# Kernel optimization log

Measured on AMD Instinct MI355X. Metric: run time of the kernel, lower is better.

Reference implementation:

```python
import jax, jax.numpy as jnp
import numpy as np

IN_FEATURES = 5000
N0, N1, N2 = 512, 512, 256   # num_nodes
NUM_T = 16                   # num_treatments
BATCH = 16384


def setup_inputs() -> dict:
    key = jax.random.key(0)
    ks = jax.random.split(key, 16)
    s = lambda fan_in: 1.0 / np.sqrt(fan_in)
    inp = {
        "input": jax.random.normal(ks[0], (BATCH, IN_FEATURES), dtype=jnp.float32),
        "treatment_and_dosages": jax.random.uniform(ks[1], (BATCH, NUM_T), dtype=jnp.float32),
        # encoder: in_features -> N0 -> N2 (ReLU, ReLU)
        "enc_w1": jax.random.normal(ks[2], (IN_FEATURES, N0), dtype=jnp.float32) * s(IN_FEATURES),
        "enc_b1": jnp.zeros((N0,), dtype=jnp.float32),
        "enc_w2": jax.random.normal(ks[3], (N0, N2), dtype=jnp.float32) * s(N0),
        "enc_b2": jnp.zeros((N2,), dtype=jnp.float32),
        # per-treatment expert: (N2+1) -> N2, ReLU
        "expert_w": jax.random.normal(ks[4], (NUM_T, N2 + 1, N2), dtype=jnp.float32) * s(N2 + 1),
        "expert_b": jnp.zeros((NUM_T, N2), dtype=jnp.float32),
        # decoder: N2 -> N1 -> N0 -> 2*in_features (ReLU, ReLU, linear)
        "dec_w1": jax.random.normal(ks[5], (N2, N1), dtype=jnp.float32) * s(N2),
        "dec_b1": jnp.zeros((N1,), dtype=jnp.float32),
        "dec_w2": jax.random.normal(ks[6], (N1, N0), dtype=jnp.float32) * s(N1),
        "dec_b2": jnp.zeros((N0,), dtype=jnp.float32),
        "dec_w3": jax.random.normal(ks[7], (N0, 2 * IN_FEATURES), dtype=jnp.float32) * s(N0),
        "dec_b3": jnp.zeros((2 * IN_FEATURES,), dtype=jnp.float32),
    }
    return inp


def reference(input, treatment_and_dosages, enc_w1, enc_b1, enc_w2, enc_b2,
              expert_w, expert_b, dec_w1, dec_b1, dec_w2, dec_b2, dec_w3, dec_b3):
    dim = input.shape[1]
    # routing: argmax over treatment columns
    treatment = jnp.argmax(treatment_and_dosages, axis=1)          # [B] int
    # shared encoder MLP
    h = jax.nn.relu(input @ enc_w1 + enc_b1)                       # [B, N0]
    embedding = jax.nn.relu(h @ enc_w2 + enc_b2)                   # [B, N2]
    # gather each row's own dosage and append as extra feature
    dose = jnp.take_along_axis(treatment_and_dosages, treatment[:, None], axis=1)  # [B,1]
    x = jnp.concatenate([embedding, dose], axis=1)                 # [B, N2+1]
    # run all experts on all tokens (dense grouped GEMM), then select per-row expert.
    # this is the vectorized equivalent of the masked gather / per-treatment MLP /
    # scatter-add loop in the torch code.
    all_out = jax.nn.relu(jnp.einsum('bi,tio->bto', x, expert_w) + expert_b)  # [B,T,N2]
    latent_rep = jnp.take_along_axis(all_out, treatment[:, None, None], axis=1)[:, 0, :]  # [B,N2]
    # decoder MLP
    d = jax.nn.relu(latent_rep @ dec_w1 + dec_b1)
    d = jax.nn.relu(d @ dec_w2 + dec_b2)
    rec = d @ dec_w3 + dec_b3                                      # [B, 2*dim]
    gene_means = rec[:, :dim]
    gene_vars = jax.nn.softplus(rec[:, dim:]) + 0.001
    gene_reconstructions2 = jnp.concatenate([gene_means, gene_vars], axis=1)
    return gene_reconstructions2, latent_rep
```

## Files before the change

kernel.cpp:

```cpp
#include <hip/hip_runtime.h>
#include <cstdint>
#include <cstddef>

#define BATCH    16384
#define INF      5000
#define KPAD_IN  5024
#define N0       512
#define N1       512
#define N2       256
#define NUM_T    16
#define XK       288
#define N3       10000
#define N3PAD    10112

typedef _Float16 f16;
typedef _Float16 f16x8 __attribute__((ext_vector_type(8)));
typedef float    f32x4 __attribute__((ext_vector_type(4)));

typedef __attribute__((address_space(1))) void gvoid;
typedef __attribute__((address_space(3))) void lvoid;

__device__ __forceinline__ void gload_lds16(const void* g, void* l) {
    __builtin_amdgcn_global_load_lds((gvoid*)g, (lvoid*)l, 16, 0, 0);
}

__device__ __forceinline__ float fast_exp2(float x) {
    float r; asm("v_exp_f32 %0, %1" : "=v"(r) : "v"(x)); return r;
}
__device__ __forceinline__ float fast_log2(float x) {
    float r; asm("v_log_f32 %0, %1" : "=v"(r) : "v"(x)); return r;
}
__device__ __forceinline__ float fast_softplus(float v) {
    float t = fast_exp2(-fabsf(v) * 1.44269504f);
    return fmaxf(v, 0.f) + 0.69314718f * fast_log2(1.f + t);
}


__global__ void cast_input_kernel(const float* __restrict__ in, f16* __restrict__ out) {
    int tid = blockIdx.x * 256 + threadIdx.x;
    int r = tid / (KPAD_IN / 8);
    int k = (tid - r * (KPAD_IN / 8)) << 3;
    if (r >= BATCH) return;
    f16x8 v;
#pragma unroll
    for (int j = 0; j < 8; j++) {
        int kk = k + j;
        float x = (kk < INF) ? in[(size_t)r * INF + kk] : 0.f;
        v[j] = (f16)x;
    }
    *(f16x8*)(out + (size_t)r * KPAD_IN + k) = v;
}

__global__ void tcast_kernel(const float* __restrict__ W, f16* __restrict__ Wt,
                             int K, int Nsrc, int Kpad, int Ndst) {
    int tid = blockIdx.x * 256 + threadIdx.x;
    int kb = Kpad >> 3;
    int n = tid / kb;
    int k = (tid - n * kb) << 3;
    if (n >= Ndst) return;
    f16x8 v;
#pragma unroll
    for (int j = 0; j < 8; j++) {
        int kk = k + j;
        float x = (kk < K && n < Nsrc) ? W[(size_t)kk * Nsrc + n] : 0.f;
        v[j] = (f16)x;
    }
    *(f16x8*)(Wt + (size_t)n * Kpad + k) = v;
}

__global__ void tcast_expert_kernel(const float* __restrict__ W, f16* __restrict__ Wt) {
    int tid = blockIdx.x * 256 + threadIdx.x;
    int nt = tid / (XK / 8);
    int k = (tid - nt * (XK / 8)) << 3;
    if (nt >= NUM_T * N2) return;
    int t = nt >> 8, n = nt & 255;
    f16x8 v;
#pragma unroll
    for (int j = 0; j < 8; j++) {
        int kk = k + j;
        float x = (kk < N2 + 1) ? W[((size_t)t * (N2 + 1) + kk) * N2 + n] : 0.f;
        v[j] = (f16)x;
    }
    *(f16x8*)(Wt + ((size_t)t * N2 + n) * XK + k) = v;
}

__global__ void treat_kernel(const float* __restrict__ td, int* __restrict__ treat,
                             f16* __restrict__ xbuf) {
    int b = blockIdx.x * 256 + threadIdx.x;
    if (b >= BATCH) return;
    const float* row = td + (size_t)b * NUM_T;
    float mx = row[0]; int mi = 0;
#pragma unroll
    for (int i = 1; i < NUM_T; i++) {
        float v = row[i];
        if (v > mx) { mx = v; mi = i; }
    }
    treat[b] = mi;
    f16* xr = xbuf + (size_t)b * XK;
    xr[256] = (f16)mx;
#pragma unroll
    for (int i = 257; i < XK; i++) xr[i] = (f16)0.f;
}


enum { EPI_F16 = 0, EPI_EXPERT = 1, EPI_DEC3 = 2 };

template <int EPI>
__global__ __launch_bounds__(256, 2)
void gemm_tpl(const f16* __restrict__ A, const f16* __restrict__ Bt,
              const float* __restrict__ bias, int K,
              f16* __restrict__ out16, int ldo,
              const int* __restrict__ treat, float* __restrict__ outf) {
    __shared__ f16 sA[128 * 32];
    __shared__ f16 sB[128 * 32];
    const int tid  = threadIdx.x;
    const int w    = tid >> 6;
    const int lane = tid & 63;
    const int lr   = lane >> 2;
    const int lc8  = (lane & 3) * 8;
    const int r0   = blockIdx.x * 128;
    const int n0   = blockIdx.y * 128;
    const int expert = (EPI == EPI_EXPERT) ? (int)blockIdx.z : 0;

    const f16* btBase = Bt;
    if (EPI == EPI_EXPERT) btBase += (size_t)expert * N2 * K;

    const f16* a0 = A      + (size_t)(r0 + w * 16 + lr) * K + lc8;
    const f16* a1 = a0 + (size_t)64 * K;
    const f16* b0 = btBase + (size_t)(n0 + w * 16 + lr) * K + lc8;
    const f16* b1 = b0 + (size_t)64 * K;
    f16* sA0 = sA + w * 512;
    f16* sA1 = sA + (w + 4) * 512;
    f16* sB0 = sB + w * 512;
    f16* sB1 = sB + (w + 4) * 512;

    f32x4 acc[4][4];
#pragma unroll
    for (int i = 0; i < 4; i++)
#pragma unroll
        for (int j = 0; j < 4; j++) acc[i][j] = (f32x4){0.f, 0.f, 0.f, 0.f};

    const int wr = (w >> 1) * 64;
    const int wc = (w & 1) * 64;
    const int fm = lane & 15;
    const int fk = (lane >> 4) * 8;

    for (int k0 = 0; k0 < K; k0 += 32) {
        __syncthreads();
        gload_lds16(a0, sA0); gload_lds16(a1, sA1);
        gload_lds16(b0, sB0); gload_lds16(b1, sB1);
        a0 += 32; a1 += 32; b0 += 32; b1 += 32;
        __syncthreads();

        f16x8 af[4], bf[4];
#pragma unroll
        for (int mi = 0; mi < 4; mi++)
            af[mi] = *(const f16x8*)(sA + (wr + mi * 16 + fm) * 32 + fk);
#pragma unroll
        for (int ni = 0; ni < 4; ni++)
            bf[ni] = *(const f16x8*)(sB + (wc + ni * 16 + fm) * 32 + fk);
#pragma unroll
        for (int mi = 0; mi < 4; mi++)
#pragma unroll
            for (int ni = 0; ni < 4; ni++)
                acc[mi][ni] = __builtin_amdgcn_mfma_f32_16x16x32_f16(
                    af[mi], bf[ni], acc[mi][ni], 0, 0, 0);
    }

    const float* bp = (EPI == EPI_EXPERT) ? bias + expert * N2 : bias;
    const int rbase = r0 + wr + ((lane >> 4) << 2);
    const int cbase = n0 + wc + fm;
#pragma unroll
    for (int mi = 0; mi < 4; mi++) {
#pragma unroll
        for (int r = 0; r < 4; r++) {
            int row = rbase + mi * 16 + r;
            if (EPI == EPI_EXPERT) {
                if (treat[row] != expert) continue;
            }
#pragma unroll
            for (int ni = 0; ni < 4; ni++) {
                int col = cbase + ni * 16;
                float v = acc[mi][ni][r] + bp[col];
                if (EPI == EPI_F16) {
                    out16[(size_t)row * ldo + col] = (f16)fmaxf(v, 0.f);
                } else if (EPI == EPI_EXPERT) {
                    v = fmaxf(v, 0.f);
                    out16[(size_t)row * N2 + col] = (f16)v;
                    outf[(size_t)row * N2 + col] = v;
                } else {
                    if (col < N3) {
                        if (col >= INF)
                            v = fast_softplus(v) + 0.001f;
                        outf[(size_t)row * N3 + col] = v;
                    }
                }
            }
        }
    }
}


extern "C" void kernel_launch(void* const* d_in, const int* in_sizes, int n_in,
                              void* d_out, int out_size, void* d_ws, size_t ws_size,
                              hipStream_t stream) {
    const float* in_x  = (const float*)d_in[0];
    const float* td    = (const float*)d_in[1];
    const float* ew1   = (const float*)d_in[2];
    const float* eb1   = (const float*)d_in[3];
    const float* ew2   = (const float*)d_in[4];
    const float* eb2   = (const float*)d_in[5];
    const float* exw   = (const float*)d_in[6];
    const float* exb   = (const float*)d_in[7];
    const float* dw1   = (const float*)d_in[8];
    const float* db1   = (const float*)d_in[9];
    const float* dw2   = (const float*)d_in[10];
    const float* db2   = (const float*)d_in[11];
    const float* dw3   = (const float*)d_in[12];
    const float* db3   = (const float*)d_in[13];
    float* out = (float*)d_out;
    float* out_latent = out + (size_t)BATCH * N3;

    size_t off = 0;
    auto carve = [&](size_t bytes) {
        size_t p = off;
        off += (bytes + 255) & ~(size_t)255;
        return p;
    };
    char* ws = (char*)d_ws;
    f16* A16   = (f16*)(ws + carve((size_t)BATCH * KPAD_IN * 2));
    f16* h1    = (f16*)(ws + carve((size_t)BATCH * N0 * 2));
    f16* xbuf  = (f16*)(ws + carve((size_t)BATCH * XK * 2));
    f16* lat16 = (f16*)(ws + carve((size_t)BATCH * N2 * 2));
    f16* d1    = (f16*)(ws + carve((size_t)BATCH * N1 * 2));
    f16* d2    = (f16*)(ws + carve((size_t)BATCH * N0 * 2));
    f16* w1t   = (f16*)(ws + carve((size_t)N0 * KPAD_IN * 2));
    f16* w2t   = (f16*)(ws + carve((size_t)N2 * 512 * 2));
    f16* wet   = (f16*)(ws + carve((size_t)NUM_T * N2 * XK * 2));
    f16* wd1t  = (f16*)(ws + carve((size_t)N1 * 256 * 2));
    f16* wd2t  = (f16*)(ws + carve((size_t)N0 * 512 * 2));
    f16* wd3t  = (f16*)(ws + carve((size_t)N3PAD * 512 * 2));
    int* treat = (int*)(ws + carve((size_t)BATCH * 4));
    (void)ws_size; (void)in_sizes; (void)n_in; (void)out_size;

    auto blocks = [](size_t threads) { return (unsigned)((threads + 255) / 256); };

    cast_input_kernel<<<blocks((size_t)BATCH * (KPAD_IN / 8)), 256, 0, stream>>>(in_x, A16);
    tcast_kernel<<<blocks((size_t)N0 * (KPAD_IN / 8)), 256, 0, stream>>>(ew1, w1t, INF, N0, KPAD_IN, N0);
    tcast_kernel<<<blocks((size_t)N2 * (512 / 8)), 256, 0, stream>>>(ew2, w2t, N0, N2, 512, N2);
    tcast_expert_kernel<<<blocks((size_t)NUM_T * N2 * (XK / 8)), 256, 0, stream>>>(exw, wet);
    tcast_kernel<<<blocks((size_t)N1 * (256 / 8)), 256, 0, stream>>>(dw1, wd1t, N2, N1, 256, N1);
    tcast_kernel<<<blocks((size_t)N0 * (512 / 8)), 256, 0, stream>>>(dw2, wd2t, N1, N0, 512, N0);
    tcast_kernel<<<blocks((size_t)N3PAD * (512 / 8)), 256, 0, stream>>>(dw3, wd3t, N0, N3, 512, N3PAD);
    treat_kernel<<<blocks(BATCH), 256, 0, stream>>>(td, treat, xbuf);

    gemm_tpl<EPI_F16><<<dim3(BATCH / 128, N0 / 128, 1), 256, 0, stream>>>(
        A16, w1t, eb1, KPAD_IN, h1, N0, nullptr, nullptr);
    gemm_tpl<EPI_F16><<<dim3(BATCH / 128, N2 / 128, 1), 256, 0, stream>>>(
        h1, w2t, eb2, 512, xbuf, XK, nullptr, nullptr);
    gemm_tpl<EPI_EXPERT><<<dim3(BATCH / 128, N2 / 128, NUM_T), 256, 0, stream>>>(
        xbuf, wet, exb, XK, lat16, N2, treat, out_latent);
    gemm_tpl<EPI_F16><<<dim3(BATCH / 128, N1 / 128, 1), 256, 0, stream>>>(
        lat16, wd1t, db1, 256, d1, N1, nullptr, nullptr);
    gemm_tpl<EPI_F16><<<dim3(BATCH / 128, N0 / 128, 1), 256, 0, stream>>>(
        d1, wd2t, db2, 512, d2, N0, nullptr, nullptr);
    gemm_tpl<EPI_DEC3><<<dim3(BATCH / 128, N3PAD / 128, 1), 256, 0, stream>>>(
        d2, wd3t, db3, 512, nullptr, 0, nullptr, out);
}
```

Measured before the change: 1.559 ms.

## Double-buffer GEMM LDS tiles, swizzle LDS layout, vectorize input cast

The GEMM main loop now uses two LDS buffers, so global-to-LDS loads for the next K-tile are issued while MFMAs run on the current one, and there is one barrier per tile instead of two. The LDS column chunk is XOR-swizzled by row to reduce bank conflicts on fragment reads. Launch bounds are raised to 4 blocks per CU, and the input cast kernel uses float4 loads where it can. Register pressure from the higher occupancy target could cause spills, and the doubled LDS use may limit residency.

Result: faster. 1.505 ms (-3.4%).

```diff
diff --git a/kernel.cpp b/kernel.cpp
--- a/kernel.cpp
+++ b/kernel.cpp
@@ -16,6 +16,7 @@
 typedef _Float16 f16;
 typedef _Float16 f16x8 __attribute__((ext_vector_type(8)));
 typedef float    f32x4 __attribute__((ext_vector_type(4)));
+typedef float    float4v __attribute__((ext_vector_type(4)));
 
 typedef __attribute__((address_space(1))) void gvoid;
 typedef __attribute__((address_space(3))) void lvoid;
@@ -42,11 +43,18 @@
     int k = (tid - r * (KPAD_IN / 8)) << 3;
     if (r >= BATCH) return;
     f16x8 v;
-#pragma unroll
-    for (int j = 0; j < 8; j++) {
-        int kk = k + j;
-        float x = (kk < INF) ? in[(size_t)r * INF + kk] : 0.f;
-        v[j] = (f16)x;
+    if (k + 8 <= INF) {
+        float4v x0 = *(const float4v*)(in + (size_t)r * INF + k);
+        float4v x1 = *(const float4v*)(in + (size_t)r * INF + k + 4);
+#pragma unroll
+        for (int j = 0; j < 4; j++) { v[j] = (f16)x0[j]; v[j + 4] = (f16)x1[j]; }
+    } else {
+#pragma unroll
+        for (int j = 0; j < 8; j++) {
+            int kk = k + j;
+            float x = (kk < INF) ? in[(size_t)r * INF + kk] : 0.f;
+            v[j] = (f16)x;
+        }
     }
     *(f16x8*)(out + (size_t)r * KPAD_IN + k) = v;
 }
@@ -106,18 +114,18 @@
 enum { EPI_F16 = 0, EPI_EXPERT = 1, EPI_DEC3 = 2 };
 
 template <int EPI>
-__global__ __launch_bounds__(256, 2)
+__global__ __launch_bounds__(256, 4)
 void gemm_tpl(const f16* __restrict__ A, const f16* __restrict__ Bt,
               const float* __restrict__ bias, int K,
               f16* __restrict__ out16, int ldo,
               const int* __restrict__ treat, float* __restrict__ outf) {
-    __shared__ f16 sA[128 * 32];
-    __shared__ f16 sB[128 * 32];
+    __shared__ f16 sA[2][128 * 32];
+    __shared__ f16 sB[2][128 * 32];
     const int tid  = threadIdx.x;
     const int w    = tid >> 6;
     const int lane = tid & 63;
     const int lr   = lane >> 2;
-    const int lc8  = (lane & 3) * 8;
+    const int lc8  = (((lane & 3) ^ (lr & 3)) << 3);
     const int r0   = blockIdx.x * 128;
     const int n0   = blockIdx.y * 128;
     const int expert = (EPI == EPI_EXPERT) ? (int)blockIdx.z : 0;
@@ -129,10 +137,7 @@
     const f16* a1 = a0 + (size_t)64 * K;
     const f16* b0 = btBase + (size_t)(n0 + w * 16 + lr) * K + lc8;
     const f16* b1 = b0 + (size_t)64 * K;
-    f16* sA0 = sA + w * 512;
-    f16* sA1 = sA + (w + 4) * 512;
-    f16* sB0 = sB + w * 512;
-    f16* sB1 = sB + (w + 4) * 512;
+    const int so = w * 512;
 
     f32x4 acc[4][4];
 #pragma unroll
@@ -143,29 +148,47 @@
     const int wr = (w >> 1) * 64;
     const int wc = (w & 1) * 64;
     const int fm = lane & 15;
-    const int fk = (lane >> 4) * 8;
-
-    for (int k0 = 0; k0 < K; k0 += 32) {
-        __syncthreads();
-        gload_lds16(a0, sA0); gload_lds16(a1, sA1);
-        gload_lds16(b0, sB0); gload_lds16(b1, sB1);
+    const int fk = (((lane >> 4) ^ (lane & 3)) << 3);
+
+    auto stage = [&](int buf) {
+        f16* bA = &sA[buf][0];
+        f16* bB = &sB[buf][0];
+        gload_lds16(a0, bA + so); gload_lds16(a1, bA + so + 2048);
+        gload_lds16(b0, bB + so); gload_lds16(b1, bB + so + 2048);
         a0 += 32; a1 += 32; b0 += 32; b1 += 32;
-        __syncthreads();
-
+    };
+    auto compute = [&](int buf) {
+        const f16* pA = &sA[buf][0];
+        const f16* pB = &sB[buf][0];
         f16x8 af[4], bf[4];
 #pragma unroll
         for (int mi = 0; mi < 4; mi++)
-            af[mi] = *(const f16x8*)(sA + (wr + mi * 16 + fm) * 32 + fk);
+            af[mi] = *(const f16x8*)(pA + (wr + mi * 16 + fm) * 32 + fk);
 #pragma unroll
         for (int ni = 0; ni < 4; ni++)
-            bf[ni] = *(const f16x8*)(sB + (wc + ni * 16 + fm) * 32 + fk);
+            bf[ni] = *(const f16x8*)(pB + (wc + ni * 16 + fm) * 32 + fk);
 #pragma unroll
         for (int mi = 0; mi < 4; mi++)
 #pragma unroll
             for (int ni = 0; ni < 4; ni++)
                 acc[mi][ni] = __builtin_amdgcn_mfma_f32_16x16x32_f16(
                     af[mi], bf[ni], acc[mi][ni], 0, 0, 0);
-    }
+    };
+
+    const int nt = K >> 5;
+    stage(0);
+    __syncthreads();
+    int t = 0;
+    while (t + 2 <= nt) {
+        stage(1);
+        compute(0);
+        __syncthreads();
+        if (t + 2 < nt) stage(0);
+        compute(1);
+        __syncthreads();
+        t += 2;
+    }
+    if (t < nt) compute(0);
 
     const float* bp = (EPI == EPI_EXPERT) ? bias + expert * N2 : bias;
     const int rbase = r0 + wr + ((lane >> 4) << 2);
```
